# Kernel tuning notes

Hardware: AMD Instinct MI355X
Metric: run time of the kernel (lower is better)

## Reference

```python
import jax, jax.numpy as jnp
import numpy as np

B, N, C = 2, 2048, 512
H = 8
HD = C // H


def _xavier(key, shape):
    fan_in, fan_out = shape[-1], shape[-2] if len(shape) > 1 else shape[-1]
    limit = float(np.sqrt(6.0 / (fan_in + fan_out)))
    return jax.random.uniform(key, shape, jnp.float32, -limit, limit)


def setup_inputs() -> dict:
    key = jax.random.key(0)
    ks = jax.random.split(key, 8)
    return {
        "x": jax.random.normal(ks[0], (B, N, C), jnp.float32),
        "pos_embedding": jax.random.normal(ks[1], (B, N, C), jnp.float32),
        "Wqkv": _xavier(ks[2], (3 * C, C)),      # nn.Linear(dim, 3*dim, bias=False)
        "Wpos": _xavier(ks[3], (C, C)),          # pos_proj, bias=False
        "u_bias": _xavier(ks[4], (H, HD)),
        "v_bias": _xavier(ks[5], (H, HD)),
        "Wproj": _xavier(ks[6], (C, C)),
        "bproj": jnp.zeros((C,), jnp.float32),
    }


def _relative_shift(ps):
    # ps: [B, H, N, M]
    b, h, n, m = ps.shape
    ps = jnp.pad(ps, ((0, 0), (0, 0), (0, 0), (1, 0)))  # zero column in front
    ps = ps.reshape(b, h, m + 1, n)[:, :, 1:, :]
    return ps.reshape(b, h, n, m)


def reference(x, pos_embedding, Wqkv, Wpos, u_bias, v_bias, Wproj, bproj):
    b, n, c = x.shape
    scale = HD ** -0.5
    qkv = (x @ Wqkv.T).reshape(b, n, 3, H, HD)
    q = qkv[:, :, 0].transpose(0, 2, 1, 3)  # [B,H,N,HD]
    k = qkv[:, :, 1].transpose(0, 2, 1, 3)
    v = qkv[:, :, 2].transpose(0, 2, 1, 3)
    pos = (pos_embedding @ Wpos.T).reshape(b, -1, H, HD)  # [B,M,H,HD]

    # content score: (q + u_bias) @ k^T -> [B,H,N,N]
    content = jnp.einsum("bhnd,bhmd->bhnm", q + u_bias[None, :, None, :], k)
    # pos score: (q + v_bias) @ pos^T -> [B,H,N,M]
    pos_score = jnp.einsum("bhnd,bmhd->bhnm", q + v_bias[None, :, None, :], pos)
    pos_score = _relative_shift(pos_score)

    attn = jax.nn.softmax((pos_score + content) * scale, axis=-1)
    out = jnp.einsum("bhnm,bhmd->bhnd", attn, v)
    out = out.transpose(0, 2, 1, 3).reshape(b, n, c)
    return out @ Wproj.T + bproj
```

## Files before the change

kernel.cpp:

```cpp
#include <hip/hip_runtime.h>
#include <hip/hip_bf16.h>

typedef __attribute__((ext_vector_type(8))) short bf16x8;
typedef __attribute__((ext_vector_type(4))) short bf16x4;
typedef __attribute__((ext_vector_type(4))) float f32x4;

__device__ __forceinline__ float bf2f(unsigned short u) {
  union { unsigned int i; float f; } c; c.i = ((unsigned int)u) << 16; return c.f;
}
__device__ __forceinline__ unsigned short f2bf(float x) {
  __hip_bfloat16 h = __float2bfloat16(x);
  unsigned short u;
  __builtin_memcpy(&u, &h, 2);
  return u;
}
__device__ __forceinline__ unsigned int pk2(float a, float b) {
  return (unsigned int)f2bf(a) | ((unsigned int)f2bf(b) << 16);
}

__device__ __forceinline__ uint4 ld8f(const float* p) {
  const float4 a = *(const float4*)p;
  const float4 b = *(const float4*)(p + 4);
  uint4 r;
  r.x = pk2(a.x, a.y);
  r.y = pk2(a.z, a.w);
  r.z = pk2(b.x, b.y);
  r.w = pk2(b.z, b.w);
  return r;
}

__device__ __forceinline__ void gload16(const unsigned short* g, short* l) {
  __builtin_amdgcn_global_load_lds((const __attribute__((address_space(1))) void*)g,
                                   (__attribute__((address_space(3))) void*)l, 16, 0, 0);
}

__global__ __launch_bounds__(256) void k_cvt(const float* __restrict__ x,
    const float* __restrict__ pe, const float* __restrict__ wq,
    const float* __restrict__ wp, const float* __restrict__ wj,
    unsigned short* __restrict__ dst) {
  const long long i8 = ((long long)blockIdx.x * 256 + threadIdx.x) * 8;
  const float* src; long long off;
  if (i8 < 2097152)      { src = x;  off = i8; }
  else if (i8 < 4194304) { src = pe; off = i8 - 2097152; }
  else if (i8 < 4980736) { src = wq; off = i8 - 4194304; }
  else if (i8 < 5242880) { src = wp; off = i8 - 4980736; }
  else                   { src = wj; off = i8 - 5242880; }
  *(uint4*)&dst[i8] = ld8f(src + off);
}

__device__ __forceinline__ void gemm128_mainloop(const unsigned short* __restrict__ Arow,
                                                 const unsigned short* __restrict__ Wrow,
                                                 short* Asl, short* Wsl, f32x4 acc[4][4]) {
  const int tid = threadIdx.x, w = tid >> 6, lane = tid & 63, lm = lane & 15, lq = lane >> 4;
  const int wm = w >> 1, wn = w & 1;
  const int lrow = lane >> 3;
  const int gcol = (((lane & 7) ^ lrow) * 8);
#pragma unroll
  for (int mt = 0; mt < 4; ++mt)
#pragma unroll
    for (int nt = 0; nt < 4; ++nt) acc[mt][nt] = (f32x4){0.f, 0.f, 0.f, 0.f};
#pragma unroll 1
  for (int kc = 0; kc < 512; kc += 64) {
    __syncthreads();
#pragma unroll
    for (int ld = 0; ld < 4; ++ld) {
      const int rbase = w * 32 + ld * 8;
      gload16(&Arow[(size_t)(rbase + lrow) * 512 + kc + gcol], &Asl[rbase * 64]);
      gload16(&Wrow[(size_t)(rbase + lrow) * 512 + kc + gcol], &Wsl[rbase * 64]);
    }
    __syncthreads();
#pragma unroll
    for (int kk = 0; kk < 2; ++kk) {
      const int pcs = ((kk * 4 + lq) ^ (lm & 7)) * 8;
      bf16x8 af[4], bfr[4];
#pragma unroll
      for (int mt = 0; mt < 4; ++mt)
        af[mt] = *(const bf16x8*)&Asl[(wm * 64 + mt * 16 + lm) * 64 + pcs];
#pragma unroll
      for (int nt = 0; nt < 4; ++nt)
        bfr[nt] = *(const bf16x8*)&Wsl[(wn * 64 + nt * 16 + lm) * 64 + pcs];
#pragma unroll
      for (int mt = 0; mt < 4; ++mt)
#pragma unroll
        for (int nt = 0; nt < 4; ++nt)
          acc[mt][nt] = __builtin_amdgcn_mfma_f32_16x16x32_bf16(af[mt], bfr[nt], acc[mt][nt], 0, 0, 0);
    }
  }
}

__device__ __forceinline__ void epi_rows(const f32x4 acc[4][4], const float* __restrict__ bias,
                                         short* TT, unsigned short* __restrict__ dst,
                                         int m0, int cc0) {
  const int tid = threadIdx.x, w = tid >> 6, lane = tid & 63, lm = lane & 15, lq = lane >> 4;
  const int wm = w >> 1, wn = w & 1;
  __syncthreads();
#pragma unroll
  for (int mt = 0; mt < 4; ++mt)
#pragma unroll
    for (int nt = 0; nt < 4; ++nt) {
      const int ccl = wn * 64 + nt * 16 + lm;
      const float bb = bias ? bias[(cc0 + ccl) & 511] : 0.f;
#pragma unroll
      for (int r = 0; r < 4; ++r)
        TT[(wm * 64 + mt * 16 + lq * 4 + r) * 130 + ccl] = (short)f2bf(acc[mt][nt][r] + bb);
    }
  __syncthreads();
#pragma unroll
  for (int rr = 0; rr < 8; ++rr) {
    const int ml = rr * 16 + (tid >> 4), ccl = (tid & 15) * 8;
    const uint4 v = *(const uint4*)&TT[ml * 130 + ccl];
    const int m = m0 + ml, b = m >> 11, n = m & 2047;
    const int cc = cc0 + ccl, hh = (cc >> 6) & 7, d = cc & 63;
    *(uint4*)&dst[((size_t)(b * 8 + hh) * 2048 + n) * 64 + d] = v;
  }
}

__device__ __forceinline__ void epi_cols(const f32x4 acc[4][4], short* TT,
                                         unsigned short* __restrict__ vt,
                                         int m0, int cc0) {
  const int tid = threadIdx.x, w = tid >> 6, lane = tid & 63, lm = lane & 15, lq = lane >> 4;
  const int wm = w >> 1, wn = w & 1;
  __syncthreads();
#pragma unroll
  for (int mt = 0; mt < 4; ++mt)
#pragma unroll
    for (int nt = 0; nt < 4; ++nt) {
      const int ccl = wn * 64 + nt * 16 + lm;
#pragma unroll
      for (int r = 0; r < 4; ++r)
        TT[(wm * 64 + mt * 16 + lq * 4 + r) * 130 + ccl] = (short)f2bf(acc[mt][nt][r]);
    }
  __syncthreads();
  const int b = m0 >> 11;
#pragma unroll
  for (int ss = 0; ss < 8; ++ss) {
    const int ccl = ss * 16 + (tid >> 4), mch = (tid & 15) * 8;
    alignas(16) unsigned short tmp[8];
#pragma unroll
    for (int j = 0; j < 8; ++j) tmp[j] = (unsigned short)TT[(mch + j) * 130 + ccl];
    const int cc = cc0 + ccl, hh = (cc >> 6) & 7, d = cc & 63;
    const int n = (m0 & 2047) + mch;
    *(uint4*)&vt[((size_t)(b * 8 + hh) * 64 + d) * 2048 + n] = *(const uint4*)tmp;
  }
}

__global__ __launch_bounds__(256) void k_gemm_qkvpos(const unsigned short* __restrict__ xb,
    const unsigned short* __restrict__ peb, const unsigned short* __restrict__ wqb,
    const unsigned short* __restrict__ wpb, const float* __restrict__ ub,
    const float* __restrict__ vb, unsigned short* __restrict__ qu,
    unsigned short* __restrict__ qv, unsigned short* __restrict__ kg,
    unsigned short* __restrict__ vt, unsigned short* __restrict__ pos) {
  __shared__ short SB[16640];
  f32x4 acc[4][4];
  const int m0 = blockIdx.y * 128, cc0 = blockIdx.x * 128;
  const unsigned short* Arow = (cc0 < 1536 ? xb : peb) + (size_t)m0 * 512;
  const unsigned short* Wrow = (cc0 < 1536) ? (wqb + (size_t)cc0 * 512)
                                            : (wpb + (size_t)(cc0 - 1536) * 512);
  gemm128_mainloop(Arow, Wrow, SB, SB + 8192, acc);
  const int sec = cc0 >> 9;
  if (sec == 0) {
    epi_rows(acc, ub, SB, qu, m0, cc0);
    epi_rows(acc, vb, SB, qv, m0, cc0);
  } else if (sec == 1) {
    epi_rows(acc, nullptr, SB, kg, m0, cc0);
  } else if (sec == 2) {
    epi_cols(acc, SB, vt, m0, cc0);
  } else {
    epi_rows(acc, nullptr, SB, pos, m0, cc0);
  }
}

__global__ __launch_bounds__(512, 4) void k_flash(const unsigned short* __restrict__ qu,
    const unsigned short* __restrict__ qv, const unsigned short* __restrict__ kg,
    const unsigned short* __restrict__ vt, const unsigned short* __restrict__ posg,
    unsigned short* __restrict__ og) {
  __shared__ short SB[30036];
  short* KsB = SB;
  short* VsB = SB + 8192;
  short* Pn  = SB + 16384;
  short* T   = SB + 24576;
  float* Ored = (float*)SB;
  const int tid = threadIdx.x, w = tid >> 6, lane = tid & 63, lm = lane & 15, lq = lane >> 4;
  const int wk = w & 3;
  const int h  = w >> 2;
  const int sw = w >> 1;
  const int ph = w & 1;
  const int hw = blockIdx.x + 32 * blockIdx.y;
  const int xcd = hw & 7, idx = hw >> 3;
  const int bh = xcd * 2 + (idx & 1);
  const int i0 = (idx >> 1) * 64;
  const size_t bhs = (size_t)bh;
  const unsigned short* qub = qu + bhs * (2048 * 64);
  const unsigned short* qvb = qv + bhs * (2048 * 64);
  const unsigned short* pob = posg + bhs * (2048 * 64);
  const int x7 = lm & 7;
  const int kc0 = (lq ^ x7) * 8, kc1 = ((lq + 4) ^ x7) * 8;
  const int xe = (lm + 7) & 7;
  const int ec0 = (lq ^ xe) * 8, ec1 = ((lq + 4) ^ xe) * 8;
  const int ve = (((2 * wk + (lq >> 1)) ^ x7) * 8) + (lq & 1) * 4;
  const int r0c0 = (lq ^ 7) * 8, r0c1 = ((lq + 4) ^ 7) * 8;
  const int lrow = lane >> 3;
  const int gcol = ((lane & 7) ^ lrow) * 8;
  const unsigned short* ksrc = &kg[(bhs * 2048 + 8 * w + lrow) * 64 + gcol];
  const unsigned short* vsrc = &vt[(bhs * 64 + 8 * w + lrow) * 2048 + gcol];
  bf16x8 au[2][2];
#pragma unroll
  for (int qt = 0; qt < 2; ++qt) {
    const int qs = h * 2 + qt;
    au[qt][0] = *(const bf16x8*)&qub[(size_t)(i0 + qs * 16 + lm) * 64 + lq * 8];
    au[qt][1] = *(const bf16x8*)&qub[(size_t)(i0 + qs * 16 + lm) * 64 + 32 + lq * 8];
  }
  const bf16x8 av0 = *(const bf16x8*)&qvb[(size_t)(i0 + sw * 16 + lm) * 64 + lq * 8];
  const bf16x8 av1 = *(const bf16x8*)&qvb[(size_t)(i0 + sw * 16 + lm) * 64 + 32 + lq * 8];
  const int rowe = min(i0 + 49 + lm, 2047);
  const bf16x8 ae0 = *(const bf16x8*)&qvb[(size_t)rowe * 64 + lq * 8];
  const bf16x8 ae1 = *(const bf16x8*)&qvb[(size_t)rowe * 64 + 32 + lq * 8];
  float lsum[2] = {0.f, 0.f};
  f32x4 oacc[2][4];
#pragma unroll
  for (int ii = 0; ii < 2; ++ii)
#pragma unroll
    for (int jj = 0; jj < 4; ++jj) oacc[ii][jj] = (f32x4){0.f, 0.f, 0.f, 0.f};
  const int pb0 = 1983 - i0;
  gload16(ksrc, &KsB[w * 512]);
  gload16(vsrc, &VsB[w * 512]);
#pragma unroll
  for (int s = 0; s < 2; ++s) {
    const int u = 2 * w + s;
    const int slotb = (pb0 + 1 + 8 * u) & 127;
    const int grow = (pb0 + 1 + 8 * u + lrow + 4096) & 2047;
    gload16(&pob[(size_t)grow * 64 + gcol], &Pn[slotb * 64]);
  }
  bf16x8 eb0 = {}, eb1 = {};
  if (w == 1 && lm == 0) {
    const int g0 = (pb0 + 4096) & 2047;
    eb0 = *(const bf16x8*)&pob[(size_t)g0 * 64 + lq * 8];
    eb1 = *(const bf16x8*)&pob[(size_t)g0 * 64 + 32 + lq * 8];
  }
#pragma unroll 1
  for (int jt = 0; jt < 32; ++jt) {
    const int j0 = jt * 64;
    const int pb = pb0 + j0;
    const int nb = jt & 1;
    short* Ks = KsB + nb * 4096;
    short* Vs = VsB + nb * 4096;
    __syncthreads();
    if (jt < 31) {
      const int jn = j0 + 64;
      gload16(ksrc + (size_t)jn * 64, &KsB[(nb ^ 1) * 4096 + w * 512]);
      gload16(vsrc + jn, &VsB[(nb ^ 1) * 4096 + w * 512]);
    }
    const bf16x8 k0 = *(const bf16x8*)&Ks[(wk * 16 + lm) * 64 + kc0];
    const bf16x8 k1 = *(const bf16x8*)&Ks[(wk * 16 + lm) * 64 + kc1];
    f32x4 cacc[2];
#pragma unroll
    for (int qt = 0; qt < 2; ++qt) {
      cacc[qt] = __builtin_amdgcn_mfma_f32_16x16x32_bf16(k0, au[qt][0], (f32x4){0.f,0.f,0.f,0.f}, 0, 0, 0);
      cacc[qt] = __builtin_amdgcn_mfma_f32_16x16x32_bf16(k1, au[qt][1], cacc[qt], 0, 0, 0);
    }
    const int sbase = 49 - sw * 16;
    if (ph == 0) {
#pragma unroll
      for (int ct = 0; ct < 3; ++ct) {
        const int slot = (pb + sbase + ct * 16 + lm) & 127;
        const bf16x8 b0 = *(const bf16x8*)&Pn[slot * 64 + kc0];
        const bf16x8 b1 = *(const bf16x8*)&Pn[slot * 64 + kc1];
        f32x4 t0 = __builtin_amdgcn_mfma_f32_16x16x32_bf16(b0, av0, (f32x4){0.f,0.f,0.f,0.f}, 0, 0, 0);
        t0 = __builtin_amdgcn_mfma_f32_16x16x32_bf16(b1, av1, t0, 0, 0, 0);
        uint2 pk; pk.x = pk2(t0[0], t0[1]); pk.y = pk2(t0[2], t0[3]);
        *(uint2*)&T[(sw * 16 + lm) * 84 + ct * 16 + lq * 4] = pk;
      }
    } else {
#pragma unroll
      for (int ct = 3; ct < 5; ++ct) {
        const int slot = (pb + sbase + ct * 16 + lm) & 127;
        const bf16x8 b0 = *(const bf16x8*)&Pn[slot * 64 + kc0];
        const bf16x8 b1 = *(const bf16x8*)&Pn[slot * 64 + kc1];
        f32x4 t0 = __builtin_amdgcn_mfma_f32_16x16x32_bf16(b0, av0, (f32x4){0.f,0.f,0.f,0.f}, 0, 0, 0);
        t0 = __builtin_amdgcn_mfma_f32_16x16x32_bf16(b1, av1, t0, 0, 0, 0);
        uint2 pk; pk.x = pk2(t0[0], t0[1]); pk.y = pk2(t0[2], t0[3]);
        *(uint2*)&T[(sw * 16 + lm) * 84 + ct * 16 + lq * 4] = pk;
      }
      {
        bf16x8 b0, b1;
        if (sw == 0 && lm == 0) {
          b0 = eb0; b1 = eb1;
        } else {
          const int slot = (pb + sw * 16 + lm) & 127;
          b0 = *(const bf16x8*)&Pn[slot * 64 + ec0];
          b1 = *(const bf16x8*)&Pn[slot * 64 + ec1];
        }
        f32x4 e0 = __builtin_amdgcn_mfma_f32_16x16x32_bf16(b0, ae0, (f32x4){0.f,0.f,0.f,0.f}, 0, 0, 0);
        e0 = __builtin_amdgcn_mfma_f32_16x16x32_bf16(b1, ae1, e0, 0, 0, 0);
        if (lm == 15) {
          uint2 pk; pk.x = pk2(e0[0], e0[1]); pk.y = pk2(e0[2], e0[3]);
          *(uint2*)&T[64 * 84 + sw * 16 + lq * 4] = pk;
        }
        if (sw == 0 && lm == 0) {
          const int sl = (pb + 64) & 127;
          eb0 = *(const bf16x8*)&Pn[sl * 64 + r0c0];
          eb1 = *(const bf16x8*)&Pn[sl * 64 + r0c1];
        }
      }
    }
    __syncthreads();
    if (jt < 31) {
      const int slotb = (pb + 129 + 8 * w) & 127;
      const int grow = (pb + 129 + 8 * w + lrow + 4096) & 2047;
      gload16(&pob[(size_t)grow * 64 + gcol], &Pn[slotb * 64]);
    }
    const int diag = i0 - j0;
    const int jl0 = wk * 16 + lq * 4;
    bf16x4 pf[2];
    if (diag >= 64 || diag <= -128) {
      const int du = (diag <= -128) ? 1 : 0;
      const int rm = lm + du;
#pragma unroll
      for (int qt = 0; qt < 2; ++qt) {
        const int rowa = (h * 2 + qt) * 16 + rm;
        const int base = (rowa == 64) ? (64 * 84 + jl0)
                                      : (rowa * 84 + 15 + jl0 - (rm & 15));
#pragma unroll
        for (int r = 0; r < 4; ++r) {
          const float pv = bf2f((unsigned short)T[base + r]);
          const float p = exp2f((cacc[qt][r] + pv) * 0.18033688f);
          lsum[qt] += p;
          pf[qt][r] = (short)f2bf(p);
        }
      }
    } else {
#pragma unroll
      for (int qt = 0; qt < 2; ++qt) {
        const int qs = h * 2 + qt;
#pragma unroll
        for (int r = 0; r < 4; ++r) {
          const int jl = jl0 + r;
          const int d = (j0 - i0) + jl - (qs * 16 + lm);
          float pv;
          if (d == 1) {
            pv = 0.f;
          } else {
            const int rm2 = lm + ((d > 1) ? 1 : 0);
            const int rowa = qs * 16 + rm2;
            const int base = (rowa == 64) ? (64 * 84 + jl)
                                          : (rowa * 84 + 15 + jl - (rm2 & 15));
            pv = bf2f((unsigned short)T[base]);
          }
          const float p = exp2f((cacc[qt][r] + pv) * 0.18033688f);
          lsum[qt] += p;
          pf[qt][r] = (short)f2bf(p);
        }
      }
    }
#pragma unroll
    for (int dt = 0; dt < 4; ++dt) {
      const bf16x4 vf = *(const bf16x4*)&Vs[(dt * 16 + lm) * 64 + ve];
      oacc[0][dt] = __builtin_amdgcn_mfma_f32_16x16x16bf16_1k(pf[0], vf, oacc[0][dt], 0, 0, 0);
      oacc[1][dt] = __builtin_amdgcn_mfma_f32_16x16x16bf16_1k(pf[1], vf, oacc[1][dt], 0, 0, 0);
    }
  }
#pragma unroll
  for (int qt = 0; qt < 2; ++qt) {
    lsum[qt] += __shfl_xor(lsum[qt], 16, 64);
    lsum[qt] += __shfl_xor(lsum[qt], 32, 64);
  }
  __syncthreads();
  if (wk == 0) {
#pragma unroll
    for (int qt = 0; qt < 2; ++qt) {
      const int qc = (h * 2 + qt) * 16;
#pragma unroll
      for (int dt = 0; dt < 4; ++dt)
        *(f32x4*)&Ored[(dt * 16 + lm) * 68 + qc + lq * 4] = oacc[qt][dt];
      if (lq == 0) Ored[64 * 68 + qc + lm] = lsum[qt];
    }
  }
  __syncthreads();
#pragma unroll 1
  for (int r = 1; r < 4; ++r) {
    if (wk == r) {
#pragma unroll
      for (int qt = 0; qt < 2; ++qt) {
        const int qc = (h * 2 + qt) * 16;
#pragma unroll
        for (int dt = 0; dt < 4; ++dt) {
          f32x4 o = *(const f32x4*)&Ored[(dt * 16 + lm) * 68 + qc + lq * 4];
          o += oacc[qt][dt];
          *(f32x4*)&Ored[(dt * 16 + lm) * 68 + qc + lq * 4] = o;
        }
        if (lq == 0) Ored[64 * 68 + qc + lm] += lsum[qt];
      }
    }
    __syncthreads();
  }
  if (w < 4) {
    const int b = bh >> 3, hh = bh & 7;
    const f32x4 lv = *(const f32x4*)&Ored[64 * 68 + w * 16 + lq * 4];
    f32x4 inv;
#pragma unroll
    for (int r = 0; r < 4; ++r) inv[r] = 1.f / lv[r];
#pragma unroll
    for (int dt = 0; dt < 4; ++dt) {
      const f32x4 o = *(const f32x4*)&Ored[(dt * 16 + lm) * 68 + w * 16 + lq * 4];
#pragma unroll
      for (int r = 0; r < 4; ++r)
        og[((size_t)b * 2048 + i0 + w * 16 + lq * 4 + r) * 512 + hh * 64 + dt * 16 + lm] =
            f2bf(o[r] * inv[r]);
    }
  }
}

__global__ __launch_bounds__(256) void k_gemm_proj(const unsigned short* __restrict__ og,
    const unsigned short* __restrict__ wjb, const float* __restrict__ bproj,
    float* __restrict__ out) {
  __shared__ short Asl[64 * 64], Wsl[128 * 64];
  f32x4 acc[4][2];
  const int m0 = blockIdx.y * 64, cc0 = blockIdx.x * 128;
  const unsigned short* Arow = og + (size_t)m0 * 512;
  const unsigned short* Wrow = wjb + (size_t)cc0 * 512;
  const int tid = threadIdx.x, w = tid >> 6, lane = tid & 63, lm = lane & 15, lq = lane >> 4;
  const int lrow = lane >> 3;
  const int gcol = (((lane & 7) ^ lrow) * 8);
#pragma unroll
  for (int mt = 0; mt < 4; ++mt)
#pragma unroll
    for (int nt = 0; nt < 2; ++nt) acc[mt][nt] = (f32x4){0.f, 0.f, 0.f, 0.f};
#pragma unroll 1
  for (int kc = 0; kc < 512; kc += 64) {
    __syncthreads();
#pragma unroll
    for (int ld = 0; ld < 2; ++ld) {
      const int rbase = w * 16 + ld * 8;
      gload16(&Arow[(size_t)(rbase + lrow) * 512 + kc + gcol], &Asl[rbase * 64]);
    }
#pragma unroll
    for (int ld = 0; ld < 4; ++ld) {
      const int rbase = w * 32 + ld * 8;
      gload16(&Wrow[(size_t)(rbase + lrow) * 512 + kc + gcol], &Wsl[rbase * 64]);
    }
    __syncthreads();
#pragma unroll
    for (int kk = 0; kk < 2; ++kk) {
      const int pcs = ((kk * 4 + lq) ^ (lm & 7)) * 8;
      bf16x8 af[4], bfr[2];
#pragma unroll
      for (int mt = 0; mt < 4; ++mt)
        af[mt] = *(const bf16x8*)&Asl[(mt * 16 + lm) * 64 + pcs];
#pragma unroll
      for (int nt = 0; nt < 2; ++nt)
        bfr[nt] = *(const bf16x8*)&Wsl[(w * 32 + nt * 16 + lm) * 64 + pcs];
#pragma unroll
      for (int mt = 0; mt < 4; ++mt)
#pragma unroll
        for (int nt = 0; nt < 2; ++nt)
          acc[mt][nt] = __builtin_amdgcn_mfma_f32_16x16x32_bf16(af[mt], bfr[nt], acc[mt][nt], 0, 0, 0);
    }
  }
#pragma unroll
  for (int nt = 0; nt < 2; ++nt) {
    const int cc = cc0 + w * 32 + nt * 16 + lm;
    const float bias = bproj[cc];
#pragma unroll
    for (int mt = 0; mt < 4; ++mt) {
#pragma unroll
      for (int r = 0; r < 4; ++r) {
        const int m = m0 + mt * 16 + lq * 4 + r;
        out[(size_t)m * 512 + cc] = acc[mt][nt][r] + bias;
      }
    }
  }
}

extern "C" void kernel_launch(void* const* d_in, const int* in_sizes, int n_in,
                              void* d_out, int out_size, void* d_ws, size_t ws_size,
                              hipStream_t stream) {
  const float* x     = (const float*)d_in[0];
  const float* pe    = (const float*)d_in[1];
  const float* wqkv  = (const float*)d_in[2];
  const float* wpos  = (const float*)d_in[3];
  const float* ub    = (const float*)d_in[4];
  const float* vb    = (const float*)d_in[5];
  const float* wproj = (const float*)d_in[6];
  const float* bproj = (const float*)d_in[7];
  float* out = (float*)d_out;
  unsigned short* ws = (unsigned short*)d_ws;

  const size_t SZ = (size_t)2 * 8 * 2048 * 64;
  unsigned short* qu   = ws;
  unsigned short* qv   = qu + SZ;
  unsigned short* kg   = qv + SZ;
  unsigned short* vt   = kg + SZ;
  unsigned short* pos  = vt + SZ;
  unsigned short* og   = pos + SZ;
  unsigned short* cvtb = og + SZ;
  unsigned short* xb   = cvtb;
  unsigned short* peb  = cvtb + 2097152;
  unsigned short* wqb  = cvtb + 4194304;
  unsigned short* wpb  = cvtb + 4980736;
  unsigned short* wjb  = cvtb + 5242880;

  dim3 blk(256);
  hipLaunchKernelGGL(k_cvt,         dim3(2688),   blk, 0, stream, x, pe, wqkv, wpos, wproj, cvtb);
  hipLaunchKernelGGL(k_gemm_qkvpos, dim3(16, 32), blk, 0, stream,
                     xb, peb, wqb, wpb, ub, vb, qu, qv, kg, vt, pos);
  hipLaunchKernelGGL(k_flash,       dim3(32, 16), dim3(512), 0, stream, qu, qv, kg, vt, pos, og);
  hipLaunchKernelGGL(k_gemm_proj,   dim3(4, 64),  blk, 0, stream, og, wjb, bproj, out);
}
```

Measured before the change: 193.6 us.

## Double-buffer LDS tiles in QKV/pos and projection GEMM mainloops

Both GEMM kernels now split shared memory into two buffers. The tile for the next k-step is prefetched with global_load_lds while MFMAs run on the current tile, and each k-iteration needs one barrier instead of two. This is meant to hide global-to-LDS latency behind matrix math. In exchange, shared memory per block grows (64 KB in the QKV kernel), which may cut how many blocks fit on a CU.

```diff
diff --git a/kernel.cpp b/kernel.cpp
--- a/kernel.cpp
+++ b/kernel.cpp
@@ -48,46 +48,6 @@
   *(uint4*)&dst[i8] = ld8f(src + off);
 }
 
-__device__ __forceinline__ void gemm128_mainloop(const unsigned short* __restrict__ Arow,
-                                                 const unsigned short* __restrict__ Wrow,
-                                                 short* Asl, short* Wsl, f32x4 acc[4][4]) {
-  const int tid = threadIdx.x, w = tid >> 6, lane = tid & 63, lm = lane & 15, lq = lane >> 4;
-  const int wm = w >> 1, wn = w & 1;
-  const int lrow = lane >> 3;
-  const int gcol = (((lane & 7) ^ lrow) * 8);
-#pragma unroll
-  for (int mt = 0; mt < 4; ++mt)
-#pragma unroll
-    for (int nt = 0; nt < 4; ++nt) acc[mt][nt] = (f32x4){0.f, 0.f, 0.f, 0.f};
-#pragma unroll 1
-  for (int kc = 0; kc < 512; kc += 64) {
-    __syncthreads();
-#pragma unroll
-    for (int ld = 0; ld < 4; ++ld) {
-      const int rbase = w * 32 + ld * 8;
-      gload16(&Arow[(size_t)(rbase + lrow) * 512 + kc + gcol], &Asl[rbase * 64]);
-      gload16(&Wrow[(size_t)(rbase + lrow) * 512 + kc + gcol], &Wsl[rbase * 64]);
-    }
-    __syncthreads();
-#pragma unroll
-    for (int kk = 0; kk < 2; ++kk) {
-      const int pcs = ((kk * 4 + lq) ^ (lm & 7)) * 8;
-      bf16x8 af[4], bfr[4];
-#pragma unroll
-      for (int mt = 0; mt < 4; ++mt)
-        af[mt] = *(const bf16x8*)&Asl[(wm * 64 + mt * 16 + lm) * 64 + pcs];
-#pragma unroll
-      for (int nt = 0; nt < 4; ++nt)
-        bfr[nt] = *(const bf16x8*)&Wsl[(wn * 64 + nt * 16 + lm) * 64 + pcs];
-#pragma unroll
-      for (int mt = 0; mt < 4; ++mt)
-#pragma unroll
-        for (int nt = 0; nt < 4; ++nt)
-          acc[mt][nt] = __builtin_amdgcn_mfma_f32_16x16x32_bf16(af[mt], bfr[nt], acc[mt][nt], 0, 0, 0);
-    }
-  }
-}
-
 __device__ __forceinline__ void epi_rows(const f32x4 acc[4][4], const float* __restrict__ bias,
                                          short* TT, unsigned short* __restrict__ dst,
                                          int m0, int cc0) {
@@ -150,13 +110,58 @@
     const float* __restrict__ vb, unsigned short* __restrict__ qu,
     unsigned short* __restrict__ qv, unsigned short* __restrict__ kg,
     unsigned short* __restrict__ vt, unsigned short* __restrict__ pos) {
-  __shared__ short SB[16640];
+  __shared__ short SB[32768];
   f32x4 acc[4][4];
   const int m0 = blockIdx.y * 128, cc0 = blockIdx.x * 128;
   const unsigned short* Arow = (cc0 < 1536 ? xb : peb) + (size_t)m0 * 512;
   const unsigned short* Wrow = (cc0 < 1536) ? (wqb + (size_t)cc0 * 512)
                                             : (wpb + (size_t)(cc0 - 1536) * 512);
-  gemm128_mainloop(Arow, Wrow, SB, SB + 8192, acc);
+  const int tid = threadIdx.x, w = tid >> 6, lane = tid & 63, lm = lane & 15, lq = lane >> 4;
+  const int wm = w >> 1, wn = w & 1;
+  const int lrow = lane >> 3;
+  const int gcol = (((lane & 7) ^ lrow) * 8);
+#pragma unroll
+  for (int mt = 0; mt < 4; ++mt)
+#pragma unroll
+    for (int nt = 0; nt < 4; ++nt) acc[mt][nt] = (f32x4){0.f, 0.f, 0.f, 0.f};
+#pragma unroll
+  for (int ld = 0; ld < 4; ++ld) {
+    const int rbase = w * 32 + ld * 8;
+    gload16(&Arow[(size_t)(rbase + lrow) * 512 + gcol], &SB[rbase * 64]);
+    gload16(&Wrow[(size_t)(rbase + lrow) * 512 + gcol], &SB[8192 + rbase * 64]);
+  }
+#pragma unroll 1
+  for (int ks = 0; ks < 8; ++ks) {
+    short* Asl = SB + (ks & 1) * 16384;
+    short* Wsl = Asl + 8192;
+    __syncthreads();
+    if (ks < 7) {
+      const int kc = (ks + 1) * 64;
+      const int bo = ((ks & 1) ^ 1) * 16384;
+#pragma unroll
+      for (int ld = 0; ld < 4; ++ld) {
+        const int rbase = w * 32 + ld * 8;
+        gload16(&Arow[(size_t)(rbase + lrow) * 512 + kc + gcol], &SB[bo + rbase * 64]);
+        gload16(&Wrow[(size_t)(rbase + lrow) * 512 + kc + gcol], &SB[bo + 8192 + rbase * 64]);
+      }
+    }
+#pragma unroll
+    for (int kk = 0; kk < 2; ++kk) {
+      const int pcs = ((kk * 4 + lq) ^ (lm & 7)) * 8;
+      bf16x8 af[4], bfr[4];
+#pragma unroll
+      for (int mt = 0; mt < 4; ++mt)
+        af[mt] = *(const bf16x8*)&Asl[(wm * 64 + mt * 16 + lm) * 64 + pcs];
+#pragma unroll
+      for (int nt = 0; nt < 4; ++nt)
+        bfr[nt] = *(const bf16x8*)&Wsl[(wn * 64 + nt * 16 + lm) * 64 + pcs];
+#pragma unroll
+      for (int mt = 0; mt < 4; ++mt)
+#pragma unroll
+        for (int nt = 0; nt < 4; ++nt)
+          acc[mt][nt] = __builtin_amdgcn_mfma_f32_16x16x32_bf16(af[mt], bfr[nt], acc[mt][nt], 0, 0, 0);
+    }
+  }
   const int sec = cc0 >> 9;
   if (sec == 0) {
     epi_rows(acc, ub, SB, qu, m0, cc0);
@@ -413,7 +418,7 @@
 __global__ __launch_bounds__(256) void k_gemm_proj(const unsigned short* __restrict__ og,
     const unsigned short* __restrict__ wjb, const float* __restrict__ bproj,
     float* __restrict__ out) {
-  __shared__ short Asl[64 * 64], Wsl[128 * 64];
+  __shared__ short SB[24576];
   f32x4 acc[4][2];
   const int m0 = blockIdx.y * 64, cc0 = blockIdx.x * 128;
   const unsigned short* Arow = og + (size_t)m0 * 512;
@@ -425,20 +430,35 @@
   for (int mt = 0; mt < 4; ++mt)
 #pragma unroll
     for (int nt = 0; nt < 2; ++nt) acc[mt][nt] = (f32x4){0.f, 0.f, 0.f, 0.f};
+#pragma unroll
+  for (int ld = 0; ld < 2; ++ld) {
+    const int rbase = w * 16 + ld * 8;
+    gload16(&Arow[(size_t)(rbase + lrow) * 512 + gcol], &SB[rbase * 64]);
+  }
+#pragma unroll
+  for (int ld = 0; ld < 4; ++ld) {
+    const int rbase = w * 32 + ld * 8;
+    gload16(&Wrow[(size_t)(rbase + lrow) * 512 + gcol], &SB[4096 + rbase * 64]);
+  }
 #pragma unroll 1
-  for (int kc = 0; kc < 512; kc += 64) {
+  for (int ks = 0; ks < 8; ++ks) {
+    short* Asl = SB + (ks & 1) * 12288;
+    short* Wsl = Asl + 4096;
     __syncthreads();
-#pragma unroll
-    for (int ld = 0; ld < 2; ++ld) {
-      const int rbase = w * 16 + ld * 8;
-      gload16(&Arow[(size_t)(rbase + lrow) * 512 + kc + gcol], &Asl[rbase * 64]);
-    }
-#pragma unroll
-    for (int ld = 0; ld < 4; ++ld) {
-      const int rbase = w * 32 + ld * 8;
-      gload16(&Wrow[(size_t)(rbase + lrow) * 512 + kc + gcol], &Wsl[rbase * 64]);
-    }
-    __syncthreads();
+    if (ks < 7) {
+      const int kc = (ks + 1) * 64;
+      const int bo = ((ks & 1) ^ 1) * 12288;
+#pragma unroll
+      for (int ld = 0; ld < 2; ++ld) {
+        const int rbase = w * 16 + ld * 8;
+        gload16(&Arow[(size_t)(rbase + lrow) * 512 + kc + gcol], &SB[bo + rbase * 64]);
+      }
+#pragma unroll
+      for (int ld = 0; ld < 4; ++ld) {
+        const int rbase = w * 32 + ld * 8;
+        gload16(&Wrow[(size_t)(rbase + lrow) * 512 + kc + gcol], &SB[bo + 4096 + rbase * 64]);
+      }
+    }
 #pragma unroll
     for (int kk = 0; kk < 2; ++kk) {
       const int pcs = ((kk * 4 + lq) ^ (lm & 7)) * 8;
```

Measured after the change: 188.1 us. -2.8%, faster.
